# Kernel optimization log

Measured on AMD Instinct MI355X. Metric: run time of the kernel, lower is better.

The kernel has to match this reference:

```python
import jax, jax.numpy as jnp
import numpy as np

EMBED_DIM = 1024
NUM_HEADS = 16


def _mha(q_in, k_in, v_in, w_in, b_in, w_out, b_out, num_heads, mask=None):
    """torch.nn.MultiheadAttention (batch_first=True) forward, dropout=0.
    q_in: [B, Lq, E], k_in/v_in: [B, Lk, E].
    w_in: [3E, E], b_in: [3E], w_out: [E, E], b_out: [E].
    """
    E = q_in.shape[-1]
    hd = E // num_heads
    wq, wk, wv = jnp.split(w_in, 3, axis=0)
    bq, bk, bv = jnp.split(b_in, 3)
    q = q_in @ wq.T + bq
    k = k_in @ wk.T + bk
    v = v_in @ wv.T + bv
    B, Lq = q.shape[0], q.shape[1]
    Lk = k.shape[1]
    q = q.reshape(B, Lq, num_heads, hd)
    k = k.reshape(B, Lk, num_heads, hd)
    v = v.reshape(B, Lk, num_heads, hd)
    scale = 1.0 / jnp.sqrt(jnp.asarray(hd, dtype=q.dtype))
    scores = jnp.einsum('bqhd,bkhd->bhqk', q, k) * scale  # [B,H,Lq,Lk]
    if mask is not None:
        scores = scores + mask  # additive mask, broadcast over B,H
    attn = jax.nn.softmax(scores, axis=-1)
    out = jnp.einsum('bhqk,bkhd->bqhd', attn, v).reshape(B, Lq, E)
    return out @ w_out.T + b_out


def setup_inputs() -> dict:
    key = jax.random.key(0)
    ks = jax.random.split(key, 20)
    B, T, S, P, E = 4, 1024, 16, 256, EMBED_DIM
    std = 0.02
    inp = {
        'text_tokens': jax.random.normal(ks[0], (B, T, E), jnp.float32),
        'patch_groups': jax.random.normal(ks[1], (S, B, P, E), jnp.float32),
        'cls_tokens': jax.random.normal(ks[2], (B, S, E), jnp.float32),
        'int_token': jax.random.normal(ks[3], (B, 1, E), jnp.float32),
    }
    for i, name in enumerate(['text', 'patch', 'int']):
        inp[f'{name}_w_in'] = jax.random.normal(ks[4 + 4 * i], (3 * E, E), jnp.float32) * std
        inp[f'{name}_b_in'] = jnp.zeros((3 * E,), jnp.float32)
        inp[f'{name}_w_out'] = jax.random.normal(ks[5 + 4 * i], (E, E), jnp.float32) * std
        inp[f'{name}_b_out'] = jnp.zeros((E,), jnp.float32)
    return inp


def reference(text_tokens, patch_groups, cls_tokens, int_token,
              text_w_in, text_b_in, text_w_out, text_b_out,
              patch_w_in, patch_b_in, patch_w_out, patch_b_out,
              int_w_in, int_b_in, int_w_out, int_b_out):
    H = NUM_HEADS
    T = text_tokens.shape[1]
    # causal text self-attention
    causal = jnp.triu(jnp.full((T, T), -jnp.inf, dtype=text_tokens.dtype), k=1)
    text_out = _mha(text_tokens, text_tokens, text_tokens,
                    text_w_in, text_b_in, text_w_out, text_b_out, H, mask=causal)

    # per-stroke block-diagonal patch self-attention (vmapped over strokes)
    patch_self = jax.vmap(lambda p: _mha(p, p, p, patch_w_in, patch_b_in,
                                         patch_w_out, patch_b_out, H))
    patch_outs = patch_self(patch_groups)  # [S, B, P, E]

    # per-stroke CLS cross-attention over its patches (same weights)
    cls_q = jnp.swapaxes(cls_tokens, 0, 1)[:, :, None, :]  # [S, B, 1, E]
    cls_cross = jax.vmap(lambda c, p: _mha(c, p, p, patch_w_in, patch_b_in,
                                           patch_w_out, patch_b_out, H))
    cls_out = cls_cross(cls_q, patch_groups)  # [S, B, 1, E]
    cls_out = jnp.swapaxes(cls_out[:, :, 0, :], 0, 1)  # [B, S, E]

    # global INT cross-attention over [text_out ; cls_out]
    context = jnp.concatenate([text_out, cls_out], axis=1)
    int_out = _mha(int_token, context, context,
                   int_w_in, int_b_in, int_w_out, int_b_out, H)
    return (text_out, patch_outs, cls_out, int_out)
```

## Files before the change

### kernel.cpp

```cpp
#include <hip/hip_runtime.h>

typedef unsigned short u16;
typedef unsigned int u32;
typedef __attribute__((ext_vector_type(8))) short short8;
typedef __attribute__((ext_vector_type(4))) float floatx4;

#define EDIM 1024
#define H3   3072
#define HD   64

__device__ __forceinline__ float bf2f(u16 u) {
    union { u32 i; float f; } x; x.i = ((u32)u) << 16; return x.f;
}
__device__ __forceinline__ u16 f2bf(float f) {
    u32 u = __float_as_uint(f);
    u32 r = u + 0x7fffu + ((u >> 16) & 1u);
    return (u16)(r >> 16);
}

__global__ void detect_dtype(const u16* __restrict__ t, int* __restrict__ flag)
{
    __shared__ int cnt;
    if (threadIdx.x == 0) cnt = 0;
    __syncthreads();
    u16 u = t[threadIdx.x * 2];
    int e = (u >> 7) & 0xFF;
    int ok = (u == 0) || (e >= 108 && e <= 136);
    atomicAdd(&cnt, ok);
    __syncthreads();
    if (threadIdx.x == 0) flag[0] = (cnt >= 128) ? 1 : 0;
}

__global__ __launch_bounds__(256) void to_bf16_2(
    const void* __restrict__ sa, u16* __restrict__ da, int na8,
    const void* __restrict__ sb, u16* __restrict__ db, int nb8,
    const int* __restrict__ flag)
{
    int idx = blockIdx.x * 256 + threadIdx.x;
    const void* s; u16* d; long off;
    if (idx < na8) {
        s = sa; d = da; off = (long)idx * 8;
    } else {
        idx -= na8;
        if (idx >= nb8) return;
        s = sb; d = db; off = (long)idx * 8;
    }
    if (flag[0]) {
        *(uint4*)(d + off) = *(const uint4*)((const u16*)s + off);
    } else {
        const float* f = (const float*)s + off;
        float4 f0 = *(const float4*)f;
        float4 f1 = *(const float4*)(f + 4);
        uint4 p;
        p.x = (u32)f2bf(f0.x) | ((u32)f2bf(f0.y) << 16);
        p.y = (u32)f2bf(f0.z) | ((u32)f2bf(f0.w) << 16);
        p.z = (u32)f2bf(f1.x) | ((u32)f2bf(f1.y) << 16);
        p.w = (u32)f2bf(f1.z) | ((u32)f2bf(f1.w) << 16);
        *(uint4*)(d + off) = p;
    }
}

__global__ __launch_bounds__(256) void gemm_bt_bias(
    const u16* __restrict__ A, const u16* __restrict__ W,
    const u16* __restrict__ bias, u16* __restrict__ C,
    int M, int N, int K, int w_row0, int b_off)
{
    __shared__ u16 sA[128 * 64];
    __shared__ u16 sB[128 * 64];
    const int tid  = threadIdx.x;
    const int wave = tid >> 6, lane = tid & 63;

    const int MT = (M + 127) >> 7, NT = N >> 7;
    const int tpg = NT * 8;
    const int grp = blockIdx.x / tpg;
    const int rem = blockIdx.x - grp * tpg;
    int gsz = MT - grp * 8; if (gsz > 8) gsz = 8;
    const int mt = grp * 8 + rem % gsz;
    const int nt = rem / gsz;
    const int m0 = mt * 128, n0 = nt * 128;

    const int wm = (wave & 1) * 64, wn = (wave >> 1) * 64;
    const int r16 = lane & 15, q8 = (lane >> 4) * 8;
    const int lrow = lane >> 3, lcol = (lane & 7) * 8;

    floatx4 acc[4][4];
#pragma unroll
    for (int i = 0; i < 4; ++i)
#pragma unroll
        for (int j = 0; j < 4; ++j)
            acc[i][j] = (floatx4){0.f, 0.f, 0.f, 0.f};

    const u16* Wb = W + (size_t)w_row0 * K;
    for (int k0 = 0; k0 < K; k0 += 64) {
#pragma unroll
        for (int t = 0; t < 4; ++t) {
            int rr = wave * 32 + t * 8;
            int ga = m0 + rr + lrow; if (ga > M - 1) ga = M - 1;
            __builtin_amdgcn_global_load_lds(
                (const __attribute__((address_space(1))) void*)(A + (size_t)ga * K + k0 + lcol),
                (__attribute__((address_space(3))) void*)&sA[rr * 64], 16, 0, 0);
            int gb = n0 + rr + lrow; if (gb > N - 1) gb = N - 1;
            __builtin_amdgcn_global_load_lds(
                (const __attribute__((address_space(1))) void*)(Wb + (size_t)gb * K + k0 + lcol),
                (__attribute__((address_space(3))) void*)&sB[rr * 64], 16, 0, 0);
        }
        __syncthreads();
#pragma unroll
        for (int kk = 0; kk < 64; kk += 32) {
            short8 af[4], bg[4];
#pragma unroll
            for (int i = 0; i < 4; ++i)
                af[i] = *(const short8*)&sA[(wm + 16 * i + r16) * 64 + kk + q8];
#pragma unroll
            for (int j = 0; j < 4; ++j)
                bg[j] = *(const short8*)&sB[(wn + 16 * j + r16) * 64 + kk + q8];
#pragma unroll
            for (int i = 0; i < 4; ++i)
#pragma unroll
                for (int j = 0; j < 4; ++j)
                    acc[i][j] = __builtin_amdgcn_mfma_f32_16x16x32_bf16(
                        af[i], bg[j], acc[i][j], 0, 0, 0);
        }
        __syncthreads();
    }

#pragma unroll
    for (int j = 0; j < 4; ++j) {
        int col = n0 + wn + 16 * j + r16;
        float bv = bf2f(bias[b_off + col]);
#pragma unroll
        for (int i = 0; i < 4; ++i) {
            int rowb = m0 + wm + 16 * i + (lane >> 4) * 4;
#pragma unroll
            for (int r = 0; r < 4; ++r) {
                int row = rowb + r;
                if (row < M)
                    C[(size_t)row * N + col] = f2bf(acc[i][j][r] + bv);
            }
        }
    }
}

#define SLOT_U16 16384

__device__ __forceinline__ void stage_one(
    const u16* __restrict__ G, int gbase, int gmax, int K, int k2,
    const u16* ldsdst, int lane)
{
    int mm = lane ^ (lane >> 3);
    int gr = gbase + (mm >> 2); if (gr > gmax) gr = gmax;
    __builtin_amdgcn_global_load_lds(
        (const __attribute__((address_space(1))) void*)(G + (size_t)gr * K + k2 + (mm & 3) * 8),
        (__attribute__((address_space(3))) void*)ldsdst, 16, 0, 0);
}

__global__ __launch_bounds__(512, 2) void gemm256(
    const u16* __restrict__ A, const u16* __restrict__ W,
    const u16* __restrict__ bias, u16* __restrict__ C,
    int M, int N, int K, int w_row0, int b_off)
{
    __shared__ u16 lds[3 * SLOT_U16];
    const int tid = threadIdx.x;
    const int wid = tid >> 6, lane = tid & 63;

    const int MT = (M + 255) >> 8, NT = N >> 8;
    const int tpg = NT * 8;
    const int grp = blockIdx.x / tpg;
    const int rem = blockIdx.x - grp * tpg;
    int gsz = MT - grp * 8; if (gsz > 8) gsz = 8;
    const int mt = grp * 8 + rem % gsz;
    const int nt = rem / gsz;
    const int m0 = mt << 8, n0 = nt << 8;

    const int wmB = (wid >> 2) * 128;
    const int wnB = (wid & 3) * 64;
    const int r16 = lane & 15, q8 = (lane >> 4) * 8;
    const int w16 = wid * 16;
    const u16* Wb = W + (size_t)w_row0 * K;

    floatx4 acc[8][4];
#pragma unroll
    for (int i = 0; i < 8; ++i)
#pragma unroll
        for (int j = 0; j < 4; ++j)
            acc[i][j] = (floatx4){0.f, 0.f, 0.f, 0.f};

    const int KT = K >> 5;

#pragma unroll
    for (int t = 0; t < 2; ++t) {
        const int k2 = t << 5;
        const u16* sl = lds + t * SLOT_U16;
        stage_one(A,  m0 + w16,       M - 1, K, k2, sl + w16 * 32, lane);
        stage_one(A,  m0 + 128 + w16, M - 1, K, k2, sl + (128 + w16) * 32, lane);
        stage_one(Wb, n0 + w16,       N - 1, K, k2, sl + 8192 + w16 * 32, lane);
        stage_one(Wb, n0 + 128 + w16, N - 1, K, k2, sl + 8192 + (128 + w16) * 32, lane);
    }
    asm volatile("s_waitcnt vmcnt(4)" ::: "memory");
    __builtin_amdgcn_s_barrier();

    for (int t = 0; t < KT; ++t) {
        const int slot = t % 3;
        const u16* sAc = lds + slot * SLOT_U16;
        const u16* sBc = sAc + 8192;
        const int t2 = t + 2;
        const u16* sl2 = lds + (t2 % 3) * SLOT_U16;
        const int k2 = t2 << 5;
        const bool dost = t2 < KT;

        short8 bg[4];
        short8 af0[4];
#pragma unroll
        for (int i = 0; i < 4; ++i) {
            int ar = wmB + i * 16 + r16;
            int off = ar * 32 + q8;
            af0[i] = *(const short8*)&sAc[off ^ ((((u32)off >> 6) & 7) << 3)];
        }
#pragma unroll
        for (int j = 0; j < 4; ++j) {
            int br = wnB + j * 16 + r16;
            int off = br * 32 + q8;
            bg[j] = *(const short8*)&sBc[off ^ ((((u32)off >> 6) & 7) << 3)];
        }
        if (dost) {
            stage_one(A, m0 + w16,       M - 1, K, k2, sl2 + w16 * 32, lane);
            stage_one(A, m0 + 128 + w16, M - 1, K, k2, sl2 + (128 + w16) * 32, lane);
        }
        __builtin_amdgcn_s_barrier();
        __builtin_amdgcn_s_setprio(1);
#pragma unroll
        for (int i = 0; i < 4; ++i)
#pragma unroll
            for (int j = 0; j < 4; ++j)
                acc[i][j] = __builtin_amdgcn_mfma_f32_16x16x32_bf16(
                    af0[i], bg[j], acc[i][j], 0, 0, 0);
        __builtin_amdgcn_s_setprio(0);
        __builtin_amdgcn_s_barrier();

        short8 af1[4];
#pragma unroll
        for (int i = 0; i < 4; ++i) {
            int ar = wmB + 64 + i * 16 + r16;
            int off = ar * 32 + q8;
            af1[i] = *(const short8*)&sAc[off ^ ((((u32)off >> 6) & 7) << 3)];
        }
        if (dost) {
            stage_one(Wb, n0 + w16,       N - 1, K, k2, sl2 + 8192 + w16 * 32, lane);
            stage_one(Wb, n0 + 128 + w16, N - 1, K, k2, sl2 + 8192 + (128 + w16) * 32, lane);
        }
        __builtin_amdgcn_s_barrier();
        __builtin_amdgcn_s_setprio(1);
#pragma unroll
        for (int i = 0; i < 4; ++i)
#pragma unroll
            for (int j = 0; j < 4; ++j)
                acc[4 + i][j] = __builtin_amdgcn_mfma_f32_16x16x32_bf16(
                    af1[i], bg[j], acc[4 + i][j], 0, 0, 0);
        __builtin_amdgcn_s_setprio(0);

        if (t < KT - 1) {
            if (t == KT - 2) asm volatile("s_waitcnt vmcnt(0)" ::: "memory");
            else             asm volatile("s_waitcnt vmcnt(4)" ::: "memory");
            __builtin_amdgcn_s_barrier();
        }
    }

#pragma unroll
    for (int j = 0; j < 4; ++j) {
        int col = n0 + wnB + j * 16 + r16;
        float bv = bf2f(bias[b_off + col]);
#pragma unroll
        for (int i = 0; i < 8; ++i) {
            int rowb = m0 + wmB + i * 16 + (lane >> 4) * 4;
#pragma unroll
            for (int r = 0; r < 4; ++r) {
                int row = rowb + r;
                if (row < M)
                    C[(size_t)row * N + col] = f2bf(acc[i][j][r] + bv);
            }
        }
    }
}

__global__ __launch_bounds__(256) void attn_flash(
    const u16* __restrict__ qkv, u16* __restrict__ out, int L, int causal)
{
    __shared__ u16 sK[64 * 64];
    __shared__ u16 sVt[64 * 64];
    __shared__ u16 sP[4 * 16 * 64];
    const int tid = threadIdx.x;
    const int wave = tid >> 6, lane = tid & 63;
    const int h = blockIdx.y, g = blockIdx.z, qt = blockIdx.x;
    const size_t grow0 = (size_t)g * L;
    const int qw0 = qt * 64 + wave * 16;
    const int r16 = lane & 15, q8 = (lane >> 4) * 8;

    short8 qf0, qf1;
    {
        const u16* qp = qkv + (grow0 + qw0 + r16) * (size_t)H3 + h * HD + q8;
        qf0 = *(const short8*)qp;
        qf1 = *(const short8*)(qp + 32);
    }

    floatx4 o_acc[4];
#pragma unroll
    for (int dg = 0; dg < 4; ++dg) o_acc[dg] = (floatx4){0.f, 0.f, 0.f, 0.f};
    float m_r[4], l_r[4];
#pragma unroll
    for (int r = 0; r < 4; ++r) { m_r[r] = -3.0e38f; l_r[r] = 0.f; }

    u16* sPw = sP + wave * 1024;
    const int nch = causal ? (qt + 1) : (L >> 6);

    for (int c = 0; c < nch; ++c) {
        const int k0 = c * 64;
        __syncthreads();
#pragma unroll
        for (int t = 0; t < 2; ++t) {
            int idx = t * 256 + tid;
            int r = idx >> 3, c8 = (idx & 7) * 8;
            const u16* kp = qkv + (grow0 + k0 + r) * (size_t)H3 + EDIM + h * HD + c8;
            *(uint4*)&sK[r * 64 + c8] = *(const uint4*)kp;
            uint4 vw = *(const uint4*)(kp + EDIM);
            u32 vu[4] = {vw.x, vw.y, vw.z, vw.w};
#pragma unroll
            for (int i = 0; i < 4; ++i) {
                sVt[(c8 + 2 * i) * 64 + r]     = (u16)(vu[i] & 0xffffu);
                sVt[(c8 + 2 * i + 1) * 64 + r] = (u16)(vu[i] >> 16);
            }
        }
        __syncthreads();

        float sc[4][4];
#pragma unroll
        for (int kg = 0; kg < 4; ++kg) {
            const u16* kb = &sK[(kg * 16 + r16) * 64];
            short8 kf0 = *(const short8*)(kb + q8);
            short8 kf1 = *(const short8*)(kb + 32 + q8);
            floatx4 a = (floatx4){0.f, 0.f, 0.f, 0.f};
            a = __builtin_amdgcn_mfma_f32_16x16x32_bf16(qf0, kf0, a, 0, 0, 0);
            a = __builtin_amdgcn_mfma_f32_16x16x32_bf16(qf1, kf1, a, 0, 0, 0);
#pragma unroll
            for (int r = 0; r < 4; ++r) sc[kg][r] = a[r] * 0.125f;
        }
        const bool domask = causal && (k0 + 63 > qw0);
        if (domask) {
#pragma unroll
            for (int kg = 0; kg < 4; ++kg)
#pragma unroll
                for (int r = 0; r < 4; ++r) {
                    int key = k0 + kg * 16 + r16;
                    int qg  = qw0 + (lane >> 4) * 4 + r;
                    if (key > qg) sc[kg][r] = -3.0e38f;
                }
        }
        float rmax[4];
#pragma unroll
        for (int r = 0; r < 4; ++r)
            rmax[r] = fmaxf(fmaxf(sc[0][r], sc[1][r]), fmaxf(sc[2][r], sc[3][r]));
#pragma unroll
        for (int m = 1; m <= 8; m <<= 1)
#pragma unroll
            for (int r = 0; r < 4; ++r)
                rmax[r] = fmaxf(rmax[r], __shfl_xor(rmax[r], m));
        float alpha[4], rsum[4];
#pragma unroll
        for (int r = 0; r < 4; ++r) {
            float mn = fmaxf(m_r[r], rmax[r]);
            alpha[r] = __expf(m_r[r] - mn);
            m_r[r] = mn; rsum[r] = 0.f;
        }
#pragma unroll
        for (int kg = 0; kg < 4; ++kg)
#pragma unroll
            for (int r = 0; r < 4; ++r) {
                float p = __expf(sc[kg][r] - m_r[r]);
                rsum[r] += p;
                sPw[((lane >> 4) * 4 + r) * 64 + kg * 16 + r16] = f2bf(p);
            }
#pragma unroll
        for (int m = 1; m <= 8; m <<= 1)
#pragma unroll
            for (int r = 0; r < 4; ++r)
                rsum[r] += __shfl_xor(rsum[r], m);
#pragma unroll
        for (int r = 0; r < 4; ++r) l_r[r] = l_r[r] * alpha[r] + rsum[r];
#pragma unroll
        for (int dg = 0; dg < 4; ++dg)
#pragma unroll
            for (int r = 0; r < 4; ++r) o_acc[dg][r] *= alpha[r];

        __asm__ volatile("" ::: "memory");

#pragma unroll
        for (int kc = 0; kc < 2; ++kc) {
            short8 pf = *(const short8*)&sPw[r16 * 64 + kc * 32 + q8];
#pragma unroll
            for (int dg = 0; dg < 4; ++dg) {
                short8 vf = *(const short8*)&sVt[(dg * 16 + r16) * 64 + kc * 32 + q8];
                o_acc[dg] = __builtin_amdgcn_mfma_f32_16x16x32_bf16(pf, vf, o_acc[dg], 0, 0, 0);
            }
        }
    }

    float inv[4];
#pragma unroll
    for (int r = 0; r < 4; ++r) inv[r] = 1.f / l_r[r];
#pragma unroll
    for (int dg = 0; dg < 4; ++dg)
#pragma unroll
        for (int r = 0; r < 4; ++r) {
            int q = qw0 + (lane >> 4) * 4 + r;
            out[(grow0 + q) * (size_t)EDIM + h * HD + dg * 16 + r16] =
                f2bf(o_acc[dg][r] * inv[r]);
        }
}

__global__ __launch_bounds__(64) void attn_cross(
    const u16* __restrict__ kv, const u16* __restrict__ qv,
    u16* __restrict__ out, int mode)
{
    const int h = blockIdx.x, gi = blockIdx.y, lane = threadIdx.x;
    int Lk, kvStride, kOff, vOff, qRow;
    size_t kvRow0;
    if (mode == 0) {
        Lk = 256; kvStride = H3; kOff = EDIM; vOff = 2 * EDIM;
        kvRow0 = (size_t)gi * 256;
        int s = gi >> 2, b = gi & 3;
        qRow = b * 16 + s;
    } else {
        Lk = 1040; kvStride = 2 * EDIM; kOff = 0; vOff = EDIM;
        kvRow0 = (size_t)gi * 1040;
        qRow = gi;
    }
    __shared__ float sq[64];
    __shared__ float sp[1040];
    sq[lane] = bf2f(qv[(size_t)qRow * EDIM + h * HD + lane]);
    __syncthreads();

    const int nt = (Lk + 63) >> 6;
    float mloc = -3.0e38f;
    for (int t = 0; t < nt; ++t) {
        int j = t * 64 + lane;
        if (j < Lk) {
            const uint4* kp = (const uint4*)(kv + (kvRow0 + j) * (size_t)kvStride + kOff + h * HD);
            float a0 = 0, a1 = 0;
#pragma unroll
            for (int tt = 0; tt < 8; ++tt) {
                uint4 w = kp[tt];
                u32 u[4] = {w.x, w.y, w.z, w.w};
#pragma unroll
                for (int i = 0; i < 4; ++i) {
                    a0 += sq[tt * 8 + i * 2]     * bf2f((u16)(u[i] & 0xffffu));
                    a1 += sq[tt * 8 + i * 2 + 1] * bf2f((u16)(u[i] >> 16));
                }
            }
            float s_ = (a0 + a1) * 0.125f;
            sp[j] = s_;
            mloc = fmaxf(mloc, s_);
        }
    }
#pragma unroll
    for (int off = 32; off; off >>= 1) mloc = fmaxf(mloc, __shfl_xor(mloc, off));
    float lsum = 0.f;
    for (int t = 0; t < nt; ++t) {
        int j = t * 64 + lane;
        if (j < Lk) { float p = __expf(sp[j] - mloc); sp[j] = p; lsum += p; }
    }
#pragma unroll
    for (int off = 32; off; off >>= 1) lsum += __shfl_xor(lsum, off);
    __syncthreads();

    float o = 0.f;
    for (int j = 0; j < Lk; ++j)
        o += sp[j] * bf2f(kv[(kvRow0 + j) * (size_t)kvStride + vOff + h * HD + lane]);
    out[(size_t)qRow * EDIM + h * HD + lane] = f2bf(o / lsum);
}

__global__ __launch_bounds__(256) void build_ctx(
    const u16* __restrict__ to, const u16* __restrict__ co, u16* __restrict__ ctx)
{
    int idx = blockIdx.x * 256 + threadIdx.x;
    int row = idx >> 7, c8 = (idx & 127) << 3;
    int b = row / 1040, t = row - b * 1040;
    const u16* src = (t < 1024)
        ? (to + ((size_t)(b * 1024 + t) * EDIM + c8))
        : (co + ((size_t)(b * 16 + (t - 1024)) * EDIM + c8));
    *(uint4*)(ctx + (size_t)row * EDIM + c8) = *(const uint4*)src;
}

__global__ __launch_bounds__(256) void emit_out(
    const u16* __restrict__ src, void* __restrict__ dst, int n8,
    const int* __restrict__ flag)
{
    int idx = blockIdx.x * 256 + threadIdx.x;
    if (idx >= n8) return;
    const u16* s = src + (size_t)idx * 8;
    if (flag[0]) {
        *(uint4*)((u16*)dst + (size_t)idx * 8) = *(const uint4*)s;
    } else {
        float4 f0, f1;
        f0.x = bf2f(s[0]); f0.y = bf2f(s[1]); f0.z = bf2f(s[2]); f0.w = bf2f(s[3]);
        f1.x = bf2f(s[4]); f1.y = bf2f(s[5]); f1.z = bf2f(s[6]); f1.w = bf2f(s[7]);
        float4* dp = (float4*)dst + (size_t)idx * 2;
        dp[0] = f0; dp[1] = f1;
    }
}

extern "C" void kernel_launch(void* const* d_in, const int* in_sizes, int n_in,
                              void* d_out, int out_size, void* d_ws, size_t ws_size,
                              hipStream_t stream)
{
    const void* text  = d_in[0];
    const void* patch = d_in[1];
    const void* cls   = d_in[2];
    const void* intok = d_in[3];
    const void* t_win  = d_in[4];  const void* t_bin  = d_in[5];
    const void* t_wout = d_in[6];  const void* t_bout = d_in[7];
    const void* p_win  = d_in[8];  const void* p_bin  = d_in[9];
    const void* p_wout = d_in[10]; const void* p_bout = d_in[11];
    const void* i_win  = d_in[12]; const void* i_bin  = d_in[13];
    const void* i_wout = d_in[14]; const void* i_bout = d_in[15];

    u16* ws = (u16*)d_ws;
    int* flag       = (int*)d_ws;
    u16* qkv_text   = ws + 64;
    u16* qkv_patch  = ws + 12582976;
    u16* attn_text  = ws + 62914624;
    u16* attn_patch = ws + 67108928;
    u16* cls_q      = ws + 83886144;
    u16* attn_cls   = ws + 83951680;

    u16* text_bf  = attn_text;
    u16* patch_bf = attn_patch;
    u16* cls_bf   = attn_cls;
    u16* int_bf   = cls_q;
    u16* WT   = qkv_patch;
    u16* WTb  = WT + 3145728;
    u16* WP   = attn_text;
    u16* WPb  = WP + 3145728;
    u16* WO1  = qkv_text;
    u16* WO1b = WO1 + 1048576;
    u16* WO2  = qkv_text + 1049600;
    u16* WO2b = WO2 + 1048576;
    u16* WI   = qkv_text + 4259840;
    u16* WIb  = WI + 3145728;
    u16* WIO  = qkv_text + 7408640;
    u16* WIOb = WIO + 1048576;
    u16* ctx      = qkv_text;
    u16* kv_int   = qkv_patch;
    u16* q_int    = qkv_patch + 8519680;
    u16* attn_int = qkv_patch + 8523776;
    u16* out_ws   = qkv_patch + 8527872;
    u16* to_ws = out_ws;
    u16* po_ws = out_ws + 4194304;
    u16* co_ws = out_ws + 20971520;
    u16* io_ws = out_ws + 21037056;

    dim3 blk(256);
    dim3 blk5(512);
    detect_dtype<<<1, blk, 0, stream>>>((const u16*)text, flag);

    to_bf16_2<<<dim3(10240), blk, 0, stream>>>(text, text_bf, 524288,
                                               patch, patch_bf, 2097152, flag);
    to_bf16_2<<<dim3(32), blk, 0, stream>>>(cls, cls_bf, 8192, cls, cls_bf, 0, flag);
    to_bf16_2<<<dim3(1538), blk, 0, stream>>>(t_win, WT, 393216, t_bin, WTb, 384, flag);

    gemm256<<<dim3(192), blk5, 0, stream>>>(text_bf, WT, WTb, qkv_text,
                                            4096, 3072, 1024, 0, 0);
    to_bf16_2<<<dim3(1538), blk, 0, stream>>>(p_win, WP, 393216, p_bin, WPb, 384, flag);
    gemm256<<<dim3(768), blk5, 0, stream>>>(patch_bf, WP, WPb, qkv_patch,
                                            16384, 3072, 1024, 0, 0);
    gemm_bt_bias<<<dim3(1 * 8), blk, 0, stream>>>(cls_bf, WP, WPb, cls_q,
                                                  64, 1024, 1024, 0, 0);

    attn_flash<<<dim3(16, 16, 4), blk, 0, stream>>>(qkv_text, attn_text, 1024, 1);
    attn_flash<<<dim3(4, 16, 64), blk, 0, stream>>>(qkv_patch, attn_patch, 256, 0);
    attn_cross<<<dim3(16, 64), dim3(64), 0, stream>>>(qkv_patch, cls_q, attn_cls, 0);

    to_bf16_2<<<dim3(513), blk, 0, stream>>>(t_wout, WO1, 131072, t_bout, WO1b, 128, flag);
    to_bf16_2<<<dim3(513), blk, 0, stream>>>(p_wout, WO2, 131072, p_bout, WO2b, 128, flag);
    to_bf16_2<<<dim3(1538), blk, 0, stream>>>(i_win, WI, 393216, i_bin, WIb, 384, flag);
    to_bf16_2<<<dim3(513), blk, 0, stream>>>(i_wout, WIO, 131072, i_bout, WIOb, 128, flag);

    gemm_bt_bias<<<dim3(32 * 8), blk, 0, stream>>>(attn_text, WO1, WO1b, to_ws,
                                                   4096, 1024, 1024, 0, 0);
    gemm256<<<dim3(256), blk5, 0, stream>>>(attn_patch, WO2, WO2b, po_ws,
                                            16384, 1024, 1024, 0, 0);
    gemm_bt_bias<<<dim3(1 * 8), blk, 0, stream>>>(attn_cls, WO2, WO2b, co_ws,
                                                  64, 1024, 1024, 0, 0);

    build_ctx<<<dim3(2080), blk, 0, stream>>>(to_ws, co_ws, ctx);
    gemm256<<<dim3(136), blk5, 0, stream>>>(ctx, WI, WIb, kv_int,
                                            4160, 2048, 1024, 1024, 1024);
    to_bf16_2<<<dim3(2), blk, 0, stream>>>(intok, int_bf, 512, intok, int_bf, 0, flag);
    gemm_bt_bias<<<dim3(1 * 8), blk, 0, stream>>>(int_bf, WI, WIb, q_int,
                                                  4, 1024, 1024, 0, 0);
    attn_cross<<<dim3(16, 4), dim3(64), 0, stream>>>(kv_int, q_int, attn_int, 1);
    gemm_bt_bias<<<dim3(1 * 8), blk, 0, stream>>>(attn_int, WIO, WIOb, io_ws,
                                                  4, 1024, 1024, 0, 0);

    emit_out<<<dim3(10274), blk, 0, stream>>>(out_ws, d_out, 2630144, flag);
}
```

Baseline: 956.7 us.

## Deepen GEMM LDS pipeline to four stages and stage epilogue through LDS

The 256x256 GEMM moves from a 3-slot to a 4-slot LDS ring, prefetching three K-steps ahead with all loads issued at loop top. This drops the two intra-iteration barriers in favour of one per iteration. The epilogue now writes the bias-added bf16 tile to LDS and then stores rows to global with 16-byte vector writes instead of scattered 2-byte stores. LDS use grows to 128KB per block, which may reduce occupancy below the two blocks per CU the launch bounds ask for. Removing the mid-iteration barriers also changes how waves stay in step.

```diff
diff --git a/kernel.cpp b/kernel.cpp
--- a/kernel.cpp
+++ b/kernel.cpp
@@ -159,7 +159,7 @@
     const u16* __restrict__ bias, u16* __restrict__ C,
     int M, int N, int K, int w_row0, int b_off)
 {
-    __shared__ u16 lds[3 * SLOT_U16];
+    __shared__ u16 lds[4 * SLOT_U16];
     const int tid = threadIdx.x;
     const int wid = tid >> 6, lane = tid & 63;
 
@@ -188,45 +188,42 @@
     const int KT = K >> 5;
 
 #pragma unroll
-    for (int t = 0; t < 2; ++t) {
-        const int k2 = t << 5;
-        const u16* sl = lds + t * SLOT_U16;
+    for (int pt = 0; pt < 3; ++pt) {
+        const int k2 = pt << 5;
+        u16* sl = lds + pt * SLOT_U16;
         stage_one(A,  m0 + w16,       M - 1, K, k2, sl + w16 * 32, lane);
         stage_one(A,  m0 + 128 + w16, M - 1, K, k2, sl + (128 + w16) * 32, lane);
         stage_one(Wb, n0 + w16,       N - 1, K, k2, sl + 8192 + w16 * 32, lane);
         stage_one(Wb, n0 + 128 + w16, N - 1, K, k2, sl + 8192 + (128 + w16) * 32, lane);
     }
-    asm volatile("s_waitcnt vmcnt(4)" ::: "memory");
+    asm volatile("s_waitcnt vmcnt(8)" ::: "memory");
+    __builtin_amdgcn_sched_barrier(0);
     __builtin_amdgcn_s_barrier();
 
     for (int t = 0; t < KT; ++t) {
-        const int slot = t % 3;
-        const u16* sAc = lds + slot * SLOT_U16;
+        const u16* sAc = lds + (t & 3) * SLOT_U16;
         const u16* sBc = sAc + 8192;
-        const int t2 = t + 2;
-        const u16* sl2 = lds + (t2 % 3) * SLOT_U16;
-        const int k2 = t2 << 5;
-        const bool dost = t2 < KT;
-
-        short8 bg[4];
-        short8 af0[4];
+
+        if (t + 3 < KT) {
+            const int k2 = (t + 3) << 5;
+            u16* sl = lds + ((t + 3) & 3) * SLOT_U16;
+            stage_one(A,  m0 + w16,       M - 1, K, k2, sl + w16 * 32, lane);
+            stage_one(A,  m0 + 128 + w16, M - 1, K, k2, sl + (128 + w16) * 32, lane);
+            stage_one(Wb, n0 + w16,       N - 1, K, k2, sl + 8192 + w16 * 32, lane);
+            stage_one(Wb, n0 + 128 + w16, N - 1, K, k2, sl + 8192 + (128 + w16) * 32, lane);
+        }
+
+        short8 af0[4], bg[4];
 #pragma unroll
         for (int i = 0; i < 4; ++i) {
-            int ar = wmB + i * 16 + r16;
-            int off = ar * 32 + q8;
+            int off = (wmB + i * 16 + r16) * 32 + q8;
             af0[i] = *(const short8*)&sAc[off ^ ((((u32)off >> 6) & 7) << 3)];
         }
 #pragma unroll
         for (int j = 0; j < 4; ++j) {
-            int br = wnB + j * 16 + r16;
-            int off = br * 32 + q8;
+            int off = (wnB + j * 16 + r16) * 32 + q8;
             bg[j] = *(const short8*)&sBc[off ^ ((((u32)off >> 6) & 7) << 3)];
         }
-        if (dost) {
-            stage_one(A, m0 + w16,       M - 1, K, k2, sl2 + w16 * 32, lane);
-            stage_one(A, m0 + 128 + w16, M - 1, K, k2, sl2 + (128 + w16) * 32, lane);
-        }
-        __builtin_amdgcn_s_barrier();
         __builtin_amdgcn_s_setprio(1);
 #pragma unroll
         for (int i = 0; i < 4; ++i)
@@ -235,20 +232,13 @@
                 acc[i][j] = __builtin_amdgcn_mfma_f32_16x16x32_bf16(
                     af0[i], bg[j], acc[i][j], 0, 0, 0);
         __builtin_amdgcn_s_setprio(0);
-        __builtin_amdgcn_s_barrier();
 
         short8 af1[4];
 #pragma unroll
         for (int i = 0; i < 4; ++i) {
-            int ar = wmB + 64 + i * 16 + r16;
-            int off = ar * 32 + q8;
+            int off = (wmB + 64 + i * 16 + r16) * 32 + q8;
             af1[i] = *(const short8*)&sAc[off ^ ((((u32)off >> 6) & 7) << 3)];
         }
-        if (dost) {
-            stage_one(Wb, n0 + w16,       N - 1, K, k2, sl2 + 8192 + w16 * 32, lane);
-            stage_one(Wb, n0 + 128 + w16, N - 1, K, k2, sl2 + 8192 + (128 + w16) * 32, lane);
-        }
-        __builtin_amdgcn_s_barrier();
         __builtin_amdgcn_s_setprio(1);
 #pragma unroll
         for (int i = 0; i < 4; ++i)
@@ -259,26 +249,36 @@
         __builtin_amdgcn_s_setprio(0);
 
         if (t < KT - 1) {
-            if (t == KT - 2) asm volatile("s_waitcnt vmcnt(0)" ::: "memory");
-            else             asm volatile("s_waitcnt vmcnt(4)" ::: "memory");
+            if (t + 3 < KT)      asm volatile("s_waitcnt vmcnt(8)" ::: "memory");
+            else if (t + 2 < KT) asm volatile("s_waitcnt vmcnt(4)" ::: "memory");
+            else                 asm volatile("s_waitcnt vmcnt(0)" ::: "memory");
+            __builtin_amdgcn_sched_barrier(0);
             __builtin_amdgcn_s_barrier();
         }
     }
 
+    __syncthreads();
+    u16* img = lds;
 #pragma unroll
     for (int j = 0; j < 4; ++j) {
-        int col = n0 + wnB + j * 16 + r16;
-        float bv = bf2f(bias[b_off + col]);
+        int col = wnB + j * 16 + r16;
+        float bv = bf2f(bias[b_off + n0 + col]);
 #pragma unroll
         for (int i = 0; i < 8; ++i) {
-            int rowb = m0 + wmB + i * 16 + (lane >> 4) * 4;
-#pragma unroll
-            for (int r = 0; r < 4; ++r) {
-                int row = rowb + r;
-                if (row < M)
-                    C[(size_t)row * N + col] = f2bf(acc[i][j][r] + bv);
-            }
-        }
+            int rowb = wmB + i * 16 + (lane >> 4) * 4;
+#pragma unroll
+            for (int r = 0; r < 4; ++r)
+                img[(rowb + r) * 256 + col] = f2bf(acc[i][j][r] + bv);
+        }
+    }
+    __syncthreads();
+#pragma unroll
+    for (int p = 0; p < 16; ++p) {
+        int r = p * 16 + (tid >> 5);
+        int c8 = (tid & 31) * 8;
+        int grow = m0 + r;
+        if (grow < M)
+            *(uint4*)&C[(size_t)grow * N + n0 + c8] = *(const uint4*)&img[r * 256 + c8];
     }
 }
 
```

Measured after the change: 887.4 us. 7.2% less time.
